# Kernel optimization log

Measured on AMD Instinct MI355X. Metric: run time of the kernel, lower is better.

The kernel has to match this reference:

```python
import jax, jax.numpy as jnp
import numpy as np

D1, D2 = 64, 64          # degree1, degree2
BW1, BW2 = 3, 3          # bandwidths
WIDTH = 64


def dst_mat(n):
    # Orthonormal DST-I matrix: self-inverse, stand-in for sp.WSWA / sp.sin_transform.
    k = np.arange(1, n + 1)
    M = np.sqrt(2.0 / (n + 1)) * np.sin(np.pi * np.outer(k, k) / (n + 1))
    return jnp.asarray(M, jnp.float32)


def transform2d(x, S_row, S_col):
    # apply spectral transform along last axis then axis -2 (T_pipe with axes [-1,-2])
    x = jnp.einsum('bcij,jk->bcik', x, S_col)
    return jnp.einsum('ki,bcij->bckj', S_row, x)


def wswano(u, w, out_ch):
    # WSWANO.forward: transform -> quasi-diag (unfold+einsum) multiply -> zero-pad -> inverse transform
    B, C, Nx, Ny = u.shape
    S1, S2 = dst_mat(Ny), dst_mat(Nx)
    a = transform2d(u, S2, S1)
    ap = a[:, :, :D1 + BW1 - 1, :D2 + BW2 - 1]
    # torch.nn.Unfold(kernel=(bw1,bw2)): patches ordered (c, ki, kj) x row-major positions
    patches = jnp.stack([ap[:, :, i:i + D1, j:j + D2]
                         for i in range(BW1) for j in range(BW2)], axis=2)  # [B,C,bw1*bw2,D1,D2]
    xp = patches.reshape(B, C * BW1 * BW2, D1 * D2)
    out = jnp.einsum('bix,iox->box', xp, w)  # quasi-diagonal spectral multiply
    b = jnp.zeros((B, out_ch, Nx, Ny), u.dtype).at[:, :, :D1, :D2].set(
        out.reshape(B, out_ch, D1, D2))
    return transform2d(b, S2, S1)  # DST-I is self-inverse => iT_pipe


def conv1x1(x, w, b):
    return jnp.einsum('bchw,oc->bohw', x, w) + b[None, :, None, None]


def gelu(x):
    return jax.nn.gelu(x, approximate=False)


def setup_inputs():
    key = jax.random.key(0)
    ks = jax.random.split(key, 18)
    B, Nx, Ny, W = 16, 128, 128, WIDTH

    def cw(k, cin, cout):
        return (2.0 / (cin + cout)) * jax.random.uniform(
            k, (cin * BW1 * BW2, cout, D1 * D2), jnp.float32)

    return {
        'x': jax.random.normal(ks[0], (B, Nx, Ny, 3), jnp.float32),
        'convl_w': cw(ks[1], 3, W - 3),
        'conv0_w': cw(ks[2], W, W),
        'conv1_w': cw(ks[3], W, W),
        'conv2_w': cw(ks[4], W, W),
        'conv3_w': cw(ks[5], W, W),
        'w0_w': 0.02 * jax.random.normal(ks[6], (W, W), jnp.float32),
        'w0_b': 0.02 * jax.random.normal(ks[7], (W,), jnp.float32),
        'w1_w': 0.02 * jax.random.normal(ks[8], (W, W), jnp.float32),
        'w1_b': 0.02 * jax.random.normal(ks[9], (W,), jnp.float32),
        'w2_w': 0.02 * jax.random.normal(ks[10], (W, W), jnp.float32),
        'w2_b': 0.02 * jax.random.normal(ks[11], (W,), jnp.float32),
        'w3_w': 0.02 * jax.random.normal(ks[12], (W, W), jnp.float32),
        'w3_b': 0.02 * jax.random.normal(ks[13], (W,), jnp.float32),
        'fc1_w': 0.02 * jax.random.normal(ks[14], (W, 128), jnp.float32),
        'fc1_b': 0.02 * jax.random.normal(ks[15], (128,), jnp.float32),
        'fc2_w': 0.02 * jax.random.normal(ks[16], (128, 1), jnp.float32),
        'fc2_b': 0.02 * jax.random.normal(ks[17], (1,), jnp.float32),
    }


def reference(x, convl_w, conv0_w, conv1_w, conv2_w, conv3_w,
              w0_w, w0_b, w1_w, w1_b, w2_w, w2_b, w3_w, w3_b,
              fc1_w, fc1_b, fc2_w, fc2_b):
    x = jnp.transpose(x, (0, 3, 1, 2))                       # [B,3,Nx,Ny]
    x = jnp.concatenate([x, gelu(wswano(x, convl_w, WIDTH - 3))], axis=1)
    for ww, wb, cw_ in ((w0_w, w0_b, conv0_w), (w1_w, w1_b, conv1_w),
                        (w2_w, w2_b, conv2_w), (w3_w, w3_b, conv3_w)):
        x = x + gelu(conv1x1(x, ww, wb) + wswano(x, cw_, WIDTH))  # skip + GELU block
    x = jnp.transpose(x, (0, 2, 3, 1))                       # [B,Nx,Ny,width]
    x = gelu(x @ fc1_w + fc1_b)
    return x @ fc2_w + fc2_b                                  # [B,Nx,Ny,1]
```

## Files before the change

kernel.cpp:

```cpp
#include <hip/hip_runtime.h>
#include <math.h>

#define NB 16
#define NN 128
#define WC 64
#define DD 64
#define NP 66

typedef float v4f __attribute__((ext_vector_type(4)));

__device__ __forceinline__ float gelu_f(float x) {
    return 0.5f * x * (1.0f + erff(x * 0.70710678118654752f));
}

__global__ void k_dst(float* __restrict__ S) {
    int idx = blockIdx.x * 256 + threadIdx.x;
    int k = idx >> 7, j = idx & 127;
    double arg = 3.14159265358979323846 * (double)((k + 1) * (j + 1)) / 129.0;
    S[idx] = (float)(sqrt(2.0 / 129.0) * sin(arg));
}

__global__ void k_tin(const float* __restrict__ in, float* __restrict__ xc) {
    int idx = blockIdx.x * 256 + threadIdx.x;
    int j = idx & 127;
    int i = (idx >> 7) & 127;
    int t = idx >> 14;
    int b = t / 3, c = t - b * 3;
    xc[(((size_t)b * WC + c) << 14) + i * 128 + j] =
        in[((size_t)(b * 128 + i) * 128 + j) * 3 + c];
}

__global__ __launch_bounds__(256) void k_tfwd66(const float* __restrict__ Xg,
                                                float* __restrict__ Yc,
                                                const float* __restrict__ Sg,
                                                int Cact) {
    __shared__ float sSt[80 * 132];
    __shared__ float sU[66 * 132];
    int bid = blockIdx.x;
    int b = bid / Cact, c = bid - b * Cact;
    const float* X = Xg + (((size_t)b * WC + c) << 14);
    int tid = threadIdx.x;
    int tx = tid & 15, ty = tid >> 4;
    for (int l = tid; l < 80 * 128; l += 256)
        sSt[(l >> 7) * 132 + (l & 127)] = Sg[l];
    float acc[8][5];
#pragma unroll
    for (int r = 0; r < 8; ++r)
#pragma unroll
        for (int q = 0; q < 5; ++q) acc[r][q] = 0.f;
    for (int jh = 0; jh < 2; ++jh) {
        __syncthreads();
        for (int l = tid; l < 8192; l += 256)
            sU[(l >> 6) * 68 + (l & 63)] = X[((l >> 6) << 7) + jh * 64 + (l & 63)];
        __syncthreads();
        for (int jj = 0; jj < 64; jj += 4) {
            float4 xv[8], sv[5];
#pragma unroll
            for (int r = 0; r < 8; ++r)
                xv[r] = *(const float4*)&sU[(ty + 16 * r) * 68 + jj];
#pragma unroll
            for (int q = 0; q < 5; ++q)
                sv[q] = *(const float4*)&sSt[(tx + 16 * q) * 132 + jh * 64 + jj];
#pragma unroll
            for (int r = 0; r < 8; ++r)
#pragma unroll
                for (int q = 0; q < 5; ++q) {
                    acc[r][q] += xv[r].x * sv[q].x;
                    acc[r][q] += xv[r].y * sv[q].y;
                    acc[r][q] += xv[r].z * sv[q].z;
                    acc[r][q] += xv[r].w * sv[q].w;
                }
        }
    }
    __syncthreads();
#pragma unroll
    for (int q = 0; q < 5; ++q) {
        int k = tx + 16 * q;
        if (k < 66) {
#pragma unroll
            for (int r = 0; r < 8; ++r)
                sU[k * 132 + ty + 16 * r] = acc[r][q];
        }
    }
    __syncthreads();
    float a2[5][5];
#pragma unroll
    for (int r = 0; r < 5; ++r)
#pragma unroll
        for (int q = 0; q < 5; ++q) a2[r][q] = 0.f;
    for (int i0 = 0; i0 < 128; i0 += 4) {
        float4 sv[5], tv[5];
#pragma unroll
        for (int r = 0; r < 5; ++r)
            sv[r] = *(const float4*)&sSt[(ty + 16 * r) * 132 + i0];
#pragma unroll
        for (int q = 0; q < 5; ++q) {
            int m = tx + 16 * q;
            if (m < 66) tv[q] = *(const float4*)&sU[m * 132 + i0];
            else { tv[q].x = 0.f; tv[q].y = 0.f; tv[q].z = 0.f; tv[q].w = 0.f; }
        }
#pragma unroll
        for (int r = 0; r < 5; ++r)
#pragma unroll
            for (int q = 0; q < 5; ++q) {
                a2[r][q] += sv[r].x * tv[q].x;
                a2[r][q] += sv[r].y * tv[q].y;
                a2[r][q] += sv[r].z * tv[q].z;
                a2[r][q] += sv[r].w * tv[q].w;
            }
    }
    float* Y = Yc + (size_t)(b * WC + c) * 4356;
#pragma unroll
    for (int r = 0; r < 5; ++r) {
        int kk = ty + 16 * r;
        if (kk < 66) {
#pragma unroll
            for (int q = 0; q < 5; ++q) {
                int m = tx + 16 * q;
                if (m < 66) Y[kk * 66 + m] = a2[r][q];
            }
        }
    }
}

__global__ __launch_bounds__(256) void k_tinv(const float* __restrict__ Op,
                                              float* __restrict__ Yg,
                                              const float* __restrict__ Sg,
                                              int Cact, int ncc, int ch_off, int do_gelu) {
    __shared__ float sS[64 * 128];
    __shared__ float sXT[64 * 132];
    int bid = blockIdx.x;
    int b = bid / Cact, c = bid - b * Cact;
    const float* X = Op + ((size_t)(b * WC + c) << 12);
    const size_t cstride = (size_t)NB * WC * 4096;
    float* Y = Yg + (((size_t)b * WC + c + ch_off) << 14);
    int tid = threadIdx.x;
    for (int l = tid; l < 8192; l += 256) sS[l] = Sg[l];
    for (int l = tid; l < 4096; l += 256) {
        int r = l >> 6, q = l & 63;
        float v = X[l];
        for (int cc = 1; cc < ncc; ++cc) v += X[cc * cstride + l];
        sXT[r * 65 + q] = v;
    }
    __syncthreads();
    int cg = tid & 7;
    int rg = tid >> 3;
    v4f a1[2][4];
#pragma unroll
    for (int r = 0; r < 2; ++r)
#pragma unroll
        for (int m = 0; m < 4; ++m) {
            a1[r][m].x = 0.f; a1[r][m].y = 0.f; a1[r][m].z = 0.f; a1[r][m].w = 0.f;
        }
    for (int j = 0; j < 64; ++j) {
        float x0 = sXT[(rg * 2 + 0) * 65 + j];
        float x1 = sXT[(rg * 2 + 1) * 65 + j];
#pragma unroll
        for (int m = 0; m < 4; ++m) {
            v4f sv = *(const v4f*)&sS[j * 128 + cg * 4 + 32 * m];
            a1[0][m] += sv * x0;
            a1[1][m] += sv * x1;
        }
    }
    __syncthreads();
#pragma unroll
    for (int r = 0; r < 2; ++r)
#pragma unroll
        for (int m = 0; m < 4; ++m)
            *(v4f*)&sXT[(rg * 2 + r) * 132 + cg * 4 + 32 * m] = a1[r][m];
    __syncthreads();
    v4f a2[4][4];
#pragma unroll
    for (int r = 0; r < 4; ++r)
#pragma unroll
        for (int m = 0; m < 4; ++m) {
            a2[r][m].x = 0.f; a2[r][m].y = 0.f; a2[r][m].z = 0.f; a2[r][m].w = 0.f;
        }
    for (int i = 0; i < 64; ++i) {
        v4f sv = *(const v4f*)&sS[i * 128 + rg * 4];
        v4f tv[4];
#pragma unroll
        for (int m = 0; m < 4; ++m)
            tv[m] = *(const v4f*)&sXT[i * 132 + cg * 4 + 32 * m];
#pragma unroll
        for (int m = 0; m < 4; ++m) {
            a2[0][m] += tv[m] * sv.x;
            a2[1][m] += tv[m] * sv.y;
            a2[2][m] += tv[m] * sv.z;
            a2[3][m] += tv[m] * sv.w;
        }
    }
#pragma unroll
    for (int r = 0; r < 4; ++r) {
        int row = rg * 4 + r;
#pragma unroll
        for (int m = 0; m < 4; ++m) {
            v4f v = a2[r][m];
            if (do_gelu) {
                v.x = gelu_f(v.x); v.y = gelu_f(v.y);
                v.z = gelu_f(v.z); v.w = gelu_f(v.w);
            }
            *(v4f*)&Y[row * 128 + cg * 4 + 32 * m] = v;
        }
    }
}

__global__ __launch_bounds__(256) void k_mix6(const float* __restrict__ Ac,
                                              const float* __restrict__ Wt,
                                              float* __restrict__ Op,
                                              int Cin, int Cout, int cper) {
    __shared__ __align__(16) float sa[2][16 * 3 * 68];
    int x = blockIdx.x;
    int ocb = blockIdx.y;
    int ccb = blockIdx.z;
    int c0 = ccb * cper;
    int c1 = c0 + cper; if (c1 > Cin) c1 = Cin;
    int tid = threadIdx.x;
    int ocl = tid & 7, yq = (tid >> 3) & 15, hf = tid >> 7;
    int oc = ocb * 8 + ocl;
    bool ocok = oc < Cout;
    int bb0 = hf * 8;
    v4f z4; z4.x = 0.f; z4.y = 0.f; z4.z = 0.f; z4.w = 0.f;

    const size_t wstep = (size_t)Cout * 4096;
    const float* wbase = Wt + (size_t)(ocok ? oc : 0) * 4096 + x * 64 + (yq << 2);

    int gidx[13], lidx[13];
#pragma unroll
    for (int k = 0; k < 13; ++k) {
        int l = tid + 256 * k;
        int lc = (l < 3168) ? l : 0;
        int bb = lc / 198; int rr = lc - bb * 198;
        int pi = rr / 66, jj = rr - pi * 66;
        gidx[k] = bb * (WC * 4356) + (x + pi) * 66 + jj;
        lidx[k] = (bb * 3 + pi) * 68 + jj;
    }
    bool k12ok = tid < 96;

    float acc[8][4];
#pragma unroll
    for (int b8 = 0; b8 < 8; ++b8)
#pragma unroll
        for (int k = 0; k < 4; ++k) acc[b8][k] = 0.f;

    {
        float sreg[13];
#pragma unroll
        for (int k = 0; k < 13; ++k) sreg[k] = Ac[(size_t)gidx[k] + (size_t)c0 * 4356];
#pragma unroll
        for (int k = 0; k < 12; ++k) sa[0][lidx[k]] = sreg[k];
        if (k12ok) sa[0][lidx[12]] = sreg[12];
    }
    v4f wvA[9];
#pragma unroll
    for (int t = 0; t < 9; ++t)
        wvA[t] = ocok ? __builtin_nontemporal_load(
                            (const v4f*)(wbase + ((size_t)c0 * 9 + t) * wstep))
                      : z4;
    __syncthreads();

    int cur = 0;
    for (int c = c0; c < c1; ++c) {
        int cn = c + 1;
        bool hn = cn < c1;
        float sreg[13];
        v4f wvN[9];
        if (hn) {
#pragma unroll
            for (int k = 0; k < 13; ++k)
                sreg[k] = Ac[(size_t)gidx[k] + (size_t)cn * 4356];
#pragma unroll
            for (int t = 0; t < 9; ++t)
                wvN[t] = ocok ? __builtin_nontemporal_load(
                                    (const v4f*)(wbase + ((size_t)cn * 9 + t) * wstep))
                              : z4;
        }
        const float* sab = sa[cur];
#pragma unroll
        for (int pi = 0; pi < 3; ++pi) {
#pragma unroll
            for (int b8 = 0; b8 < 8; ++b8) {
                const float* sp = &sab[((bb0 + b8) * 3 + pi) * 68 + (yq << 2)];
                float4 s0 = *(const float4*)sp;
                float2 s1 = *(const float2*)(sp + 4);
                float sv[6] = {s0.x, s0.y, s0.z, s0.w, s1.x, s1.y};
#pragma unroll
                for (int k = 0; k < 4; ++k)
#pragma unroll
                    for (int pj = 0; pj < 3; ++pj)
                        acc[b8][k] = fmaf(sv[k + pj], wvA[pi * 3 + pj][k], acc[b8][k]);
            }
        }
        if (hn) {
            float* san = sa[cur ^ 1];
#pragma unroll
            for (int k = 0; k < 12; ++k) san[lidx[k]] = sreg[k];
            if (k12ok) san[lidx[12]] = sreg[12];
            __syncthreads();
#pragma unroll
            for (int t = 0; t < 9; ++t) wvA[t] = wvN[t];
            cur ^= 1;
        }
    }

    if (ocok) {
        float* Opc = Op + (size_t)ccb * ((size_t)NB * WC * 4096);
#pragma unroll
        for (int b8 = 0; b8 < 8; ++b8) {
            float4 o4;
            o4.x = acc[b8][0]; o4.y = acc[b8][1];
            o4.z = acc[b8][2]; o4.w = acc[b8][3];
            *(float4*)&Opc[(((size_t)(bb0 + b8) * WC + oc) << 12) + x * 64 + (yq << 2)] = o4;
        }
    }
}

__global__ __launch_bounds__(256) void k_blockup(float* __restrict__ xc,
                                                 const float* __restrict__ sp,
                                                 const float* __restrict__ wmat,
                                                 const float* __restrict__ bias) {
    __shared__ float sw[64 * 64];
    __shared__ float sx[128 * 65];
    __shared__ float sb[64];
    int bi = blockIdx.x;
    int b = bi >> 7, i = bi & 127;
    int tid = threadIdx.x;
    for (int l = tid; l < 4096; l += 256) sw[l] = wmat[l];
    if (tid < 64) sb[tid] = bias[tid];
    for (int l = tid; l < 8192; l += 256) {
        int c = l >> 7, j = l & 127;
        sx[j * 65 + c] = xc[(((size_t)b * WC + c) << 14) + i * 128 + j];
    }
    __syncthreads();
    int j = tid & 127, h = tid >> 7;
    float xr[64];
#pragma unroll
    for (int c = 0; c < 64; ++c) xr[c] = sx[j * 65 + c];
#pragma unroll 2
    for (int o = 0; o < 32; ++o) {
        int oc = h * 32 + o;
        float a = sb[oc];
#pragma unroll
        for (int c4 = 0; c4 < 16; ++c4) {
            v4f w4 = *(const v4f*)&sw[oc * 64 + c4 * 4];
            a = fmaf(xr[c4 * 4 + 0], w4.x, a);
            a = fmaf(xr[c4 * 4 + 1], w4.y, a);
            a = fmaf(xr[c4 * 4 + 2], w4.z, a);
            a = fmaf(xr[c4 * 4 + 3], w4.w, a);
        }
        size_t gi = (((size_t)b * WC + oc) << 14) + i * 128 + j;
        float v = a + sp[gi];
        xc[gi] = sx[j * 65 + oc] + gelu_f(v);
    }
}

__global__ __launch_bounds__(256) void k_fc(const float* __restrict__ xc,
                                            const float* __restrict__ W1,
                                            const float* __restrict__ b1,
                                            const float* __restrict__ W2,
                                            const float* __restrict__ b2,
                                            float* __restrict__ out) {
    __shared__ float sW1T[128 * 68];
    __shared__ float sx[128 * 65];
    __shared__ float sW2[128];
    __shared__ float sb1[128];
    __shared__ float spart[256];
    int bi = blockIdx.x; int b = bi >> 7, i = bi & 127;
    int tid = threadIdx.x;
    for (int l = tid; l < 8192; l += 256) {
        int c = l >> 7, oo = l & 127;
        sW1T[oo * 68 + c] = W1[l];
    }
    if (tid < 128) { sW2[tid] = W2[tid]; sb1[tid] = b1[tid]; }
    for (int l = tid; l < 8192; l += 256) {
        int c = l >> 7, j = l & 127;
        sx[j * 65 + c] = xc[(((size_t)b * WC + c) << 14) + i * 128 + j];
    }
    __syncthreads();
    int j = tid & 127, h = tid >> 7;
    float xr[64];
#pragma unroll
    for (int c = 0; c < 64; ++c) xr[c] = sx[j * 65 + c];
    float part = 0.f;
#pragma unroll 2
    for (int o = 0; o < 64; ++o) {
        int oo = h * 64 + o;
        float a = sb1[oo];
#pragma unroll
        for (int c4 = 0; c4 < 16; ++c4) {
            v4f w4 = *(const v4f*)&sW1T[oo * 68 + c4 * 4];
            a = fmaf(xr[c4 * 4 + 0], w4.x, a);
            a = fmaf(xr[c4 * 4 + 1], w4.y, a);
            a = fmaf(xr[c4 * 4 + 2], w4.z, a);
            a = fmaf(xr[c4 * 4 + 3], w4.w, a);
        }
        part += gelu_f(a) * sW2[oo];
    }
    spart[j * 2 + h] = part;
    __syncthreads();
    if (h == 0) out[(size_t)bi * 128 + j] = spart[j * 2] + spart[j * 2 + 1] + b2[0];
}

extern "C" void kernel_launch(void* const* d_in, const int* in_sizes, int n_in,
                              void* d_out, int out_size, void* d_ws, size_t ws_size,
                              hipStream_t stream) {
    (void)in_sizes; (void)n_in; (void)out_size; (void)ws_size;
    const float* x_in    = (const float*)d_in[0];
    const float* convl_w = (const float*)d_in[1];
    const float* conv_w[4] = {(const float*)d_in[2], (const float*)d_in[3],
                              (const float*)d_in[4], (const float*)d_in[5]};
    const float* ww[4] = {(const float*)d_in[6], (const float*)d_in[8],
                          (const float*)d_in[10], (const float*)d_in[12]};
    const float* wb[4] = {(const float*)d_in[7], (const float*)d_in[9],
                          (const float*)d_in[11], (const float*)d_in[13]};
    const float* fc1w = (const float*)d_in[14];
    const float* fc1b = (const float*)d_in[15];
    const float* fc2w = (const float*)d_in[16];
    const float* fc2b = (const float*)d_in[17];
    float* out = (float*)d_out;

    float* S   = (float*)d_ws;
    float* xc  = S + 16384;
    float* t1  = xc + (size_t)NB * WC * 16384;
    float* tA  = t1 + (size_t)NB * WC * 16384;
    float* Op  = tA + (size_t)NB * WC * 4356;

    k_dst<<<64, 256, 0, stream>>>(S);
    k_tin<<<3072, 256, 0, stream>>>(x_in, xc);

    k_tfwd66<<<NB * 3, 256, 0, stream>>>(xc, tA, S, 3);
    k_mix6<<<dim3(64, 8, 1), 256, 0, stream>>>(tA, convl_w, Op, 3, 61, 3);
    k_tinv<<<NB * 61, 256, 0, stream>>>(Op, xc, S, 61, 1, 3, 1);

    for (int L = 0; L < 4; ++L) {
        k_tfwd66<<<NB * WC, 256, 0, stream>>>(xc, tA, S, WC);
        k_mix6<<<dim3(64, 8, 2), 256, 0, stream>>>(tA, conv_w[L], Op, WC, WC, 32);
        k_tinv<<<NB * WC, 256, 0, stream>>>(Op, t1, S, WC, 2, 0, 0);
        k_blockup<<<2048, 256, 0, stream>>>(xc, t1, ww[L], wb[L]);
    }

    k_fc<<<2048, 256, 0, stream>>>(xc, fc1w, fc1b, fc2w, fc2b, out);
}
```

Before: 1.792 ms.

## Stage mix-kernel activations via direct global-to-LDS loads with padded rows

The forward-transform output rows are padded from 66 to 68 floats so that rows are 16-byte aligned. The mixing kernel now copies activations straight into LDS with global_load_lds 16-byte transfers, replacing register staging and scalar shared stores. Each block now covers two x rows for all 16 batches (16x4 accumulators per thread) instead of one x row for half the batches, which halves the grid and adds an occupancy hint of 2. This is meant to cut load-instruction and register-staging overhead, but it raises register pressure and means the async LDS writes depend on the existing barrier for correct ordering.

```diff
diff --git a/kernel.cpp b/kernel.cpp
--- a/kernel.cpp
+++ b/kernel.cpp
@@ -8,9 +8,16 @@
 #define NP 66
 
 typedef float v4f __attribute__((ext_vector_type(4)));
+typedef unsigned int u32;
 
 __device__ __forceinline__ float gelu_f(float x) {
     return 0.5f * x * (1.0f + erff(x * 0.70710678118654752f));
+}
+
+__device__ __forceinline__ void gload16(const float* g, float* l) {
+    __builtin_amdgcn_global_load_lds(
+        (const __attribute__((address_space(1))) u32*)g,
+        (__attribute__((address_space(3))) u32*)l, 16, 0, 0);
 }
 
 __global__ void k_dst(float* __restrict__ S) {
@@ -109,7 +116,7 @@
                 a2[r][q] += sv[r].w * tv[q].w;
             }
     }
-    float* Y = Yc + (size_t)(b * WC + c) * 4356;
+    float* Y = Yc + (size_t)(b * WC + c) * 4488;
 #pragma unroll
     for (int r = 0; r < 5; ++r) {
         int kk = ty + 16 * r;
@@ -117,7 +124,7 @@
 #pragma unroll
             for (int q = 0; q < 5; ++q) {
                 int m = tx + 16 * q;
-                if (m < 66) Y[kk * 66 + m] = a2[r][q];
+                if (m < 66) Y[kk * 68 + m] = a2[r][q];
             }
         }
     }
@@ -205,51 +212,47 @@
     }
 }
 
-__global__ __launch_bounds__(256) void k_mix6(const float* __restrict__ Ac,
-                                              const float* __restrict__ Wt,
-                                              float* __restrict__ Op,
-                                              int Cin, int Cout, int cper) {
-    __shared__ __align__(16) float sa[2][16 * 3 * 68];
-    int x = blockIdx.x;
+__global__ __launch_bounds__(256, 2) void k_mix6(const float* __restrict__ Ac,
+                                                 const float* __restrict__ Wt,
+                                                 float* __restrict__ Op,
+                                                 int Cin, int Cout, int cper) {
+    __shared__ __align__(16) float sa[2][16 * 4 * 68];
+    int bx = blockIdx.x;
     int ocb = blockIdx.y;
     int ccb = blockIdx.z;
     int c0 = ccb * cper;
     int c1 = c0 + cper; if (c1 > Cin) c1 = Cin;
     int tid = threadIdx.x;
-    int ocl = tid & 7, yq = (tid >> 3) & 15, hf = tid >> 7;
+    int ocl = tid & 7, yq = (tid >> 3) & 15, xh = tid >> 7;
+    int x = bx * 2 + xh;
     int oc = ocb * 8 + ocl;
     bool ocok = oc < Cout;
-    int bb0 = hf * 8;
     v4f z4; z4.x = 0.f; z4.y = 0.f; z4.z = 0.f; z4.w = 0.f;
 
     const size_t wstep = (size_t)Cout * 4096;
     const float* wbase = Wt + (size_t)(ocok ? oc : 0) * 4096 + x * 64 + (yq << 2);
 
-    int gidx[13], lidx[13];
-#pragma unroll
-    for (int k = 0; k < 13; ++k) {
-        int l = tid + 256 * k;
-        int lc = (l < 3168) ? l : 0;
-        int bb = lc / 198; int rr = lc - bb * 198;
-        int pi = rr / 66, jj = rr - pi * 66;
-        gidx[k] = bb * (WC * 4356) + (x + pi) * 66 + jj;
-        lidx[k] = (bb * 3 + pi) * 68 + jj;
-    }
-    bool k12ok = tid < 96;
-
-    float acc[8][4];
-#pragma unroll
-    for (int b8 = 0; b8 < 8; ++b8)
-#pragma unroll
-        for (int k = 0; k < 4; ++k) acc[b8][k] = 0.f;
+    int gbase[5];
+#pragma unroll
+    for (int k = 0; k < 5; ++k) {
+        int f = 4 * tid + 1024 * k;
+        int fv = (f < 4352) ? f : 0;
+        int bb = fv / 272; int off = fv - bb * 272;
+        gbase[k] = bb * (WC * 4488) + bx * 136 + off;
+    }
+
+    float acc[16][4];
+#pragma unroll
+    for (int bb = 0; bb < 16; ++bb)
+#pragma unroll
+        for (int k = 0; k < 4; ++k) acc[bb][k] = 0.f;
 
     {
-        float sreg[13];
-#pragma unroll
-        for (int k = 0; k < 13; ++k) sreg[k] = Ac[(size_t)gidx[k] + (size_t)c0 * 4356];
-#pragma unroll
-        for (int k = 0; k < 12; ++k) sa[0][lidx[k]] = sreg[k];
-        if (k12ok) sa[0][lidx[12]] = sreg[12];
+        const float* src = Ac + (size_t)c0 * 4488;
+#pragma unroll
+        for (int k = 0; k < 4; ++k)
+            gload16(src + gbase[k], &sa[0][4 * tid + 1024 * k]);
+        if (tid < 64) gload16(src + gbase[4], &sa[0][4 * tid + 4096]);
     }
     v4f wvA[9];
 #pragma unroll
@@ -261,26 +264,27 @@
 
     int cur = 0;
     for (int c = c0; c < c1; ++c) {
-        int cn = c + 1;
-        bool hn = cn < c1;
-        float sreg[13];
+        bool hn = (c + 1) < c1;
         v4f wvN[9];
         if (hn) {
-#pragma unroll
-            for (int k = 0; k < 13; ++k)
-                sreg[k] = Ac[(size_t)gidx[k] + (size_t)cn * 4356];
+            float* dst = sa[cur ^ 1];
+            const float* src = Ac + (size_t)(c + 1) * 4488;
+#pragma unroll
+            for (int k = 0; k < 4; ++k)
+                gload16(src + gbase[k], dst + 4 * tid + 1024 * k);
+            if (tid < 64) gload16(src + gbase[4], dst + 4 * tid + 4096);
 #pragma unroll
             for (int t = 0; t < 9; ++t)
                 wvN[t] = ocok ? __builtin_nontemporal_load(
-                                    (const v4f*)(wbase + ((size_t)cn * 9 + t) * wstep))
+                                    (const v4f*)(wbase + ((size_t)(c + 1) * 9 + t) * wstep))
                               : z4;
         }
         const float* sab = sa[cur];
 #pragma unroll
         for (int pi = 0; pi < 3; ++pi) {
 #pragma unroll
-            for (int b8 = 0; b8 < 8; ++b8) {
-                const float* sp = &sab[((bb0 + b8) * 3 + pi) * 68 + (yq << 2)];
+            for (int bb = 0; bb < 16; ++bb) {
+                const float* sp = &sab[(bb * 4 + xh + pi) * 68 + (yq << 2)];
                 float4 s0 = *(const float4*)sp;
                 float2 s1 = *(const float2*)(sp + 4);
                 float sv[6] = {s0.x, s0.y, s0.z, s0.w, s1.x, s1.y};
@@ -288,14 +292,10 @@
                 for (int k = 0; k < 4; ++k)
 #pragma unroll
                     for (int pj = 0; pj < 3; ++pj)
-                        acc[b8][k] = fmaf(sv[k + pj], wvA[pi * 3 + pj][k], acc[b8][k]);
+                        acc[bb][k] = fmaf(sv[k + pj], wvA[pi * 3 + pj][k], acc[bb][k]);
             }
         }
         if (hn) {
-            float* san = sa[cur ^ 1];
-#pragma unroll
-            for (int k = 0; k < 12; ++k) san[lidx[k]] = sreg[k];
-            if (k12ok) san[lidx[12]] = sreg[12];
             __syncthreads();
 #pragma unroll
             for (int t = 0; t < 9; ++t) wvA[t] = wvN[t];
@@ -306,11 +306,11 @@
     if (ocok) {
         float* Opc = Op + (size_t)ccb * ((size_t)NB * WC * 4096);
 #pragma unroll
-        for (int b8 = 0; b8 < 8; ++b8) {
+        for (int bb = 0; bb < 16; ++bb) {
             float4 o4;
-            o4.x = acc[b8][0]; o4.y = acc[b8][1];
-            o4.z = acc[b8][2]; o4.w = acc[b8][3];
-            *(float4*)&Opc[(((size_t)(bb0 + b8) * WC + oc) << 12) + x * 64 + (yq << 2)] = o4;
+            o4.x = acc[bb][0]; o4.y = acc[bb][1];
+            o4.z = acc[bb][2]; o4.w = acc[bb][3];
+            *(float4*)&Opc[(((size_t)bb * WC + oc) << 12) + x * 64 + (yq << 2)] = o4;
         }
     }
 }
@@ -423,18 +423,18 @@
     float* xc  = S + 16384;
     float* t1  = xc + (size_t)NB * WC * 16384;
     float* tA  = t1 + (size_t)NB * WC * 16384;
-    float* Op  = tA + (size_t)NB * WC * 4356;
+    float* Op  = tA + (size_t)NB * WC * 4488;
 
     k_dst<<<64, 256, 0, stream>>>(S);
     k_tin<<<3072, 256, 0, stream>>>(x_in, xc);
 
     k_tfwd66<<<NB * 3, 256, 0, stream>>>(xc, tA, S, 3);
-    k_mix6<<<dim3(64, 8, 1), 256, 0, stream>>>(tA, convl_w, Op, 3, 61, 3);
+    k_mix6<<<dim3(32, 8, 1), 256, 0, stream>>>(tA, convl_w, Op, 3, 61, 3);
     k_tinv<<<NB * 61, 256, 0, stream>>>(Op, xc, S, 61, 1, 3, 1);
 
     for (int L = 0; L < 4; ++L) {
         k_tfwd66<<<NB * WC, 256, 0, stream>>>(xc, tA, S, WC);
-        k_mix6<<<dim3(64, 8, 2), 256, 0, stream>>>(tA, conv_w[L], Op, WC, WC, 32);
+        k_mix6<<<dim3(32, 8, 2), 256, 0, stream>>>(tA, conv_w[L], Op, WC, WC, 32);
         k_tinv<<<NB * WC, 256, 0, stream>>>(Op, t1, S, WC, 2, 0, 0);
         k_blockup<<<2048, 256, 0, stream>>>(xc, t1, ww[L], wb[L]);
     }
```

After: 1.676 ms (median of 2 runs). 6.5% less time.
